# Kernel tuning notes

Hardware: AMD Instinct MI355X
Metric: run time of the kernel (lower is better)

## Reference

```python
import jax, jax.numpy as jnp
import numpy as np

T, B, N = 1000, 64, 512
DT = 0.01
EL, VR, TR, TINF = -0.07, -0.07, -0.06, -0.05
A_VAL = 2.6239240169525146
A1_VAL = -0.015625353902578354
A2_VAL = -1.0590057373046875
B_VAL = 12.77495288848877
G_VAL = 45.24007797241211
K1, K2 = 200.0, 20.0
R1, R2 = 0.3858567178249359, -1.1421641111373901
C = 1.0


def setup_inputs() -> dict:
    key = jax.random.key(0)
    x = jax.random.normal(key, (T, B, N), dtype=jnp.float32)
    linear = jnp.ones((1, N), jnp.float32)
    a = jnp.full((1, N), A_VAL, jnp.float32)
    A1 = jnp.full((1, N), A1_VAL * C, jnp.float32)
    A2 = jnp.full((1, N), A2_VAL * C, jnp.float32)
    return {"x": x, "linear": linear, "a": a, "A1": A1, "A2": A2}


def _spike(v):
    # Heaviside step (forward of SurrGradSpike)
    return (v > 0).astype(v.dtype)


def reference(x, linear, a, A1, A2):
    G = G_VAL * C

    def step(state, xt):
        V, i1, i2, Thr = state
        i1 = i1 - K1 * i1 * DT
        i2 = i2 - K2 * i2 * DT
        V = V + DT * (linear * xt + i1 + i2 - G * (V - EL)) / C
        Thr = Thr + DT * (a * (V - EL) - B_VAL * (Thr - TINF))
        spk = _spike(V - Thr)
        i1 = (1.0 - spk) * i1 + spk * (R1 * i1 + A1)
        i2 = (1.0 - spk) * i2 + spk * (R2 * i2 + A2)
        Thr = (1.0 - spk) * Thr + spk * jnp.maximum(Thr, TR)
        V = (1.0 - spk) * V + spk * VR
        return (V, i1, i2, Thr), spk

    Bd, Nd = x.shape[1], x.shape[2]
    init = (
        jnp.full((Bd, Nd), EL, x.dtype),   # V
        jnp.zeros((Bd, Nd), x.dtype),      # i1
        jnp.zeros((Bd, Nd), x.dtype),      # i2
        jnp.full((Bd, Nd), TINF, x.dtype), # Thr
    )
    _, spikes = jax.lax.scan(step, init, x)
    return spikes  # [T, B, N] (original returns np.array of per-step spikes)
```

## Files before the change

kernel.cpp:

```cpp
#include <hip/hip_runtime.h>


#define T_STEPS 1000
#define B_DIM 64
#define N_DIM 512
#define BN (B_DIM * N_DIM)

#define K_CHUNK 20
#define NCHUNK (T_STEPS / K_CHUNK)

typedef const __attribute__((address_space(1))) void* gp_t;
typedef __attribute__((address_space(3))) void* lp_t;
typedef float f32x4 __attribute__((ext_vector_type(4)));

__device__ __forceinline__ void raw_barrier() {
    asm volatile("s_barrier" ::: "memory");
}

struct Consts {
    float k200, k20, kDT, kEL, kG, kTINF, kB, kR1, kR2, kTR;
};

__device__ __forceinline__ float mn_step_spec(
    float xt, float lin, float av, float A1v, float A2v, const Consts& K,
    float& V1, float& T1, float& tm_,
    float& i1d, float& i1r, float& i2d, float& i2r, bool& sbp)
{
#pragma clang fp contract(off)
    float a1n = i1d - (K.k200 * i1d) * K.kDT;
    float a1s = i1r - (K.k200 * i1r) * K.kDT;
    float a2n = i2d - (K.k20  * i2d) * K.kDT;
    float a2s = i2r - (K.k20  * i2r) * K.kDT;
    float p   = lin * xt;
    float qn  = p + a1n;
    float qs  = p + a1s;
    float rn  = qn + a2n;
    float rs  = qs + a2s;
    float en  = V1 - K.kEL;
    float gn  = K.kG * en;
    float sn  = rn - gn;
    float dn  = K.kDT * sn;
    float dsp = K.kDT * rs;
    float Vn  = V1 + dn;
    float Vs  = K.kEL + dsp;
    float e2n = Vn - K.kEL;
    float e2s = Vs - K.kEL;
    float un  = av * e2n;
    float us  = av * e2s;
    float wn  = T1  - K.kTINF;
    float ws  = tm_ - K.kTINF;
    float bn  = K.kB * wn;
    float bs  = K.kB * ws;
    float s2n = un - bn;
    float s2s = us - bs;
    float d2n = K.kDT * s2n;
    float d2s = K.kDT * s2s;
    float T1n = T1  + d2n;
    float T1s = tm_ + d2s;
    float dfn = Vn - T1n;
    float dfs = Vs - T1s;
    float diff = sbp ? dfs : dfn;
    V1  = sbp ? Vs  : Vn;
    T1  = sbp ? T1s : T1n;
    i1d = sbp ? a1s : a1n;
    i2d = sbp ? a2s : a2n;
    bool  sb  = diff > 0.0f;
    float spk = sb ? 1.0f : 0.0f;
    sbp = sb;
    tm_ = fmaxf(T1, K.kTR);
    i1r = (K.kR1 * i1d) + A1v;
    i2r = (K.kR2 * i2d) + A2v;
    return spk;
}

__global__ __launch_bounds__(128, 1) void mn_neuron_kernel(
    const float* __restrict__ x, const float* __restrict__ linear,
    const float* __restrict__ a, const float* __restrict__ A1,
    const float* __restrict__ A2, float* __restrict__ out)
{
#pragma clang fp contract(off)
    __shared__ float xb_buf[2][K_CHUNK][64];
    __shared__ float sb_buf[2][K_CHUNK][64];

    const int lane = threadIdx.x & 63;
    const int wid  = threadIdx.x >> 6;
    const int blk  = blockIdx.x;

    if (wid == 1) {
        const float* pl = x + (size_t)(lane >> 4) * BN
                            + (size_t)blk * 64 + (size_t)(lane & 15) * 4;
        float* outp = out + (size_t)blk * 64;

        auto issue = [&](int k) {
            const float* pc = pl + (size_t)(k * K_CHUNK) * BN;
            float* dst = &xb_buf[k & 1][0][0];
#pragma unroll
            for (int s5 = 0; s5 < K_CHUNK / 4; ++s5) {
                __builtin_amdgcn_global_load_lds(
                    (gp_t)(pc + (size_t)(s5 * 4) * BN),
                    (lp_t)(dst + s5 * 4 * 64), 16, 0, 0);
            }
        };

        const int r0 = lane >> 4;
        const int c4 = (lane & 15) * 4;
        auto flush = [&](int k) {
            const int kb = k & 1;
#pragma unroll
            for (int pz = 0; pz < K_CHUNK / 4; ++pz) {
                const int row = pz * 4 + r0;
                const f32x4 v = *reinterpret_cast<const f32x4*>(
                    &sb_buf[kb][row][c4]);
                f32x4* dp = reinterpret_cast<f32x4*>(
                    outp + (size_t)(k * K_CHUNK + row) * BN + c4);
                __builtin_nontemporal_store(v, dp);
            }
        };

        issue(0);
        asm volatile("s_waitcnt vmcnt(0)" ::: "memory");
        raw_barrier();

        for (int c = 0; c < NCHUNK; ++c) {
            if (c + 1 < NCHUNK) issue(c + 1);
            if (c >= 1)         flush(c - 1);
            asm volatile("s_waitcnt vmcnt(0) lgkmcnt(0)" ::: "memory");
            raw_barrier();
        }
        flush(NCHUNK - 1);
    } else {
        const int idx = blk * 64 + lane;
        const int n   = idx & (N_DIM - 1);

        const float lin = linear[n];
        const float av  = a[n];
        const float A1v = A1[n];
        const float A2v = A2[n];

        Consts K = {200.0f, 20.0f, 0.01f, -0.07f,
                    45.24007797241211f, -0.05f, 12.77495288848877f,
                    0.3858567178249359f, -1.1421641111373901f, -0.06f};
        asm volatile("" : "+s"(K.k200), "+s"(K.k20), "+s"(K.kDT),
                          "+s"(K.kEL), "+s"(K.kG), "+s"(K.kTINF),
                          "+s"(K.kB), "+s"(K.kR1), "+s"(K.kR2), "+s"(K.kTR));

        float V1  = K.kEL;
        float T1  = K.kTINF;
        float tm_ = fmaxf(K.kTINF, K.kTR);
        float i1d = 0.0f;
        float i1r = (K.kR1 * 0.0f) + A1v;
        float i2d = 0.0f;
        float i2r = (K.kR2 * 0.0f) + A2v;
        bool  sbp = false;

        asm volatile("s_setprio 1" ::: "memory");
        raw_barrier();

        for (int c = 0; c < NCHUNK; ++c) {
            const float* src = &xb_buf[c & 1][0][lane];
            float*       dst = &sb_buf[c & 1][0][lane];
#pragma unroll
            for (int j = 0; j < K_CHUNK; ++j) {
                float xt  = src[j * 64];
                float spk = mn_step_spec(xt, lin, av, A1v, A2v, K,
                                         V1, T1, tm_, i1d, i1r, i2d, i2r, sbp);
                dst[j * 64] = spk;
            }
            asm volatile("s_waitcnt lgkmcnt(0)" ::: "memory");
            raw_barrier();
        }
    }
}

extern "C" void kernel_launch(void* const* d_in, const int* in_sizes, int n_in,
                              void* d_out, int out_size, void* d_ws, size_t ws_size,
                              hipStream_t stream) {
    const float* x      = (const float*)d_in[0];
    const float* linear = (const float*)d_in[1];
    const float* a      = (const float*)d_in[2];
    const float* A1     = (const float*)d_in[3];
    const float* A2     = (const float*)d_in[4];
    float* out = (float*)d_out;

    mn_neuron_kernel<<<BN / 64, 128, 0, stream>>>(x, linear, a, A1, A2, out);
}
```

Baseline: 246.8 us.

## Deepen x prefetch to four buffers and restructure speculative step recurrence

The producer wave now keeps three chunks of x in flight across a four-slot LDS ring, using partial vmcnt waits instead of draining all loads every chunk. The compute wave's step is reorganized so both spike/no-spike branches for the next step are integrated right after the select, with the next x value preloaded (including across chunk boundaries). This aims to shorten the serial dependency chain per timestep and hide global load latency. It adds LDS usage and relies on careful vmcnt counting at the tail. The initial step now reads xb_buf[0] after the first barrier, which depends on the first chunk having landed.

```diff
diff --git a/kernel.cpp b/kernel.cpp
--- a/kernel.cpp
+++ b/kernel.cpp
@@ -8,6 +8,7 @@
 
 #define K_CHUNK 20
 #define NCHUNK (T_STEPS / K_CHUNK)
+#define NBUF 4
 
 typedef const __attribute__((address_space(1))) void* gp_t;
 typedef __attribute__((address_space(3))) void* lp_t;
@@ -21,55 +22,76 @@
     float k200, k20, kDT, kEL, kG, kTINF, kB, kR1, kR2, kTR;
 };
 
-__device__ __forceinline__ float mn_step_spec(
-    float xt, float lin, float av, float A1v, float A2v, const Consts& K,
-    float& V1, float& T1, float& tm_,
-    float& i1d, float& i1r, float& i2d, float& i2r, bool& sbp)
+struct Pairs {
+    float Vn, Vs;
+    float Tn, Ts;
+    float i1n, i1s;
+    float i2n, i2s;
+    bool  cn, cs;
+};
+
+__device__ __forceinline__ Pairs dual_integrate(
+    float xt, float lin, float av, const Consts& K,
+    float Vin, float i1nin, float i2nin, float Tnin,
+    float i1sin, float i2sin, float Tsin)
 {
 #pragma clang fp contract(off)
-    float a1n = i1d - (K.k200 * i1d) * K.kDT;
-    float a1s = i1r - (K.k200 * i1r) * K.kDT;
-    float a2n = i2d - (K.k20  * i2d) * K.kDT;
-    float a2s = i2r - (K.k20  * i2r) * K.kDT;
+    Pairs P;
     float p   = lin * xt;
+    float a1n = i1nin - (K.k200 * i1nin) * K.kDT;
+    float a2n = i2nin - (K.k20  * i2nin) * K.kDT;
     float qn  = p + a1n;
-    float qs  = p + a1s;
     float rn  = qn + a2n;
-    float rs  = qs + a2s;
-    float en  = V1 - K.kEL;
+    float en  = Vin - K.kEL;
     float gn  = K.kG * en;
     float sn  = rn - gn;
     float dn  = K.kDT * sn;
-    float dsp = K.kDT * rs;
-    float Vn  = V1 + dn;
-    float Vs  = K.kEL + dsp;
-    float e2n = Vn - K.kEL;
-    float e2s = Vs - K.kEL;
+    float Vpn = Vin + dn;
+    float e2n = Vpn - K.kEL;
     float un  = av * e2n;
+    float wn  = Tnin - K.kTINF;
+    float bwn = K.kB * wn;
+    float s2n = un - bwn;
+    float d2n = K.kDT * s2n;
+    float Tpn = Tnin + d2n;
+    float a1s = i1sin - (K.k200 * i1sin) * K.kDT;
+    float a2s = i2sin - (K.k20  * i2sin) * K.kDT;
+    float qs  = p + a1s;
+    float rs  = qs + a2s;
+    float ds  = K.kDT * rs;
+    float Vps = K.kEL + ds;
+    float e2s = Vps - K.kEL;
     float us  = av * e2s;
-    float wn  = T1  - K.kTINF;
-    float ws  = tm_ - K.kTINF;
-    float bn  = K.kB * wn;
-    float bs  = K.kB * ws;
-    float s2n = un - bn;
-    float s2s = us - bs;
-    float d2n = K.kDT * s2n;
+    float ws  = Tsin - K.kTINF;
+    float bws = K.kB * ws;
+    float s2s = us - bws;
     float d2s = K.kDT * s2s;
-    float T1n = T1  + d2n;
-    float T1s = tm_ + d2s;
-    float dfn = Vn - T1n;
-    float dfs = Vs - T1s;
-    float diff = sbp ? dfs : dfn;
-    V1  = sbp ? Vs  : Vn;
-    T1  = sbp ? T1s : T1n;
-    i1d = sbp ? a1s : a1n;
-    i2d = sbp ? a2s : a2n;
-    bool  sb  = diff > 0.0f;
+    float Tps = Tsin + d2s;
+    P.Vn = Vpn; P.Vs = Vps; P.Tn = Tpn; P.Ts = Tps;
+    P.i1n = a1n; P.i1s = a1s; P.i2n = a2n; P.i2s = a2s;
+    P.cn = Vpn > Tpn;
+    P.cs = Vps > Tps;
+    return P;
+}
+
+__device__ __forceinline__ float resolve_and_advance(
+    float xt1, float lin, float av, float A1v, float A2v, const Consts& K,
+    Pairs& P, bool& sbp)
+{
+#pragma clang fp contract(off)
+    bool  sb  = sbp ? P.cs : P.cn;
     float spk = sb ? 1.0f : 0.0f;
+    float V1  = sbp ? P.Vs  : P.Vn;
+    float T1  = sbp ? P.Ts  : P.Tn;
+    float i1d = sbp ? P.i1s : P.i1n;
+    float i2d = sbp ? P.i2s : P.i2n;
+    float i1r  = (K.kR1 * i1d) + A1v;
+    float i2r  = (K.kR2 * i2d) + A2v;
+    float tmax = fmaxf(T1, K.kTR);
+    P = dual_integrate(xt1, lin, av, K,
+                       V1, i1d, i2d, T1,
+                       i1r, i2r, tmax);
     sbp = sb;
-    tm_ = fmaxf(T1, K.kTR);
-    i1r = (K.kR1 * i1d) + A1v;
-    i2r = (K.kR2 * i2d) + A2v;
     return spk;
 }
 
@@ -79,7 +101,7 @@
     const float* __restrict__ A2, float* __restrict__ out)
 {
 #pragma clang fp contract(off)
-    __shared__ float xb_buf[2][K_CHUNK][64];
+    __shared__ float xb_buf[NBUF][K_CHUNK][64];
     __shared__ float sb_buf[2][K_CHUNK][64];
 
     const int lane = threadIdx.x & 63;
@@ -93,7 +115,7 @@
 
         auto issue = [&](int k) {
             const float* pc = pl + (size_t)(k * K_CHUNK) * BN;
-            float* dst = &xb_buf[k & 1][0][0];
+            float* dst = &xb_buf[k & (NBUF - 1)][0][0];
 #pragma unroll
             for (int s5 = 0; s5 < K_CHUNK / 4; ++s5) {
                 __builtin_amdgcn_global_load_lds(
@@ -117,14 +139,19 @@
             }
         };
 
-        issue(0);
-        asm volatile("s_waitcnt vmcnt(0)" ::: "memory");
+        issue(0); issue(1); issue(2);
+        asm volatile("s_waitcnt vmcnt(5)" ::: "memory");
         raw_barrier();
 
         for (int c = 0; c < NCHUNK; ++c) {
-            if (c + 1 < NCHUNK) issue(c + 1);
-            if (c >= 1)         flush(c - 1);
-            asm volatile("s_waitcnt vmcnt(0) lgkmcnt(0)" ::: "memory");
+            if (c + 3 < NCHUNK) issue(c + 3);
+            if (c <= NCHUNK - 4) {
+                asm volatile("s_waitcnt vmcnt(5)" ::: "memory");
+            } else {
+                asm volatile("s_waitcnt vmcnt(0)" ::: "memory");
+            }
+            if (c >= 1) flush(c - 1);
+            asm volatile("s_waitcnt lgkmcnt(0)" ::: "memory");
             raw_barrier();
         }
         flush(NCHUNK - 1);
@@ -144,26 +171,27 @@
                           "+s"(K.kEL), "+s"(K.kG), "+s"(K.kTINF),
                           "+s"(K.kB), "+s"(K.kR1), "+s"(K.kR2), "+s"(K.kTR));
 
-        float V1  = K.kEL;
-        float T1  = K.kTINF;
-        float tm_ = fmaxf(K.kTINF, K.kTR);
-        float i1d = 0.0f;
-        float i1r = (K.kR1 * 0.0f) + A1v;
-        float i2d = 0.0f;
-        float i2r = (K.kR2 * 0.0f) + A2v;
-        bool  sbp = false;
-
         asm volatile("s_setprio 1" ::: "memory");
         raw_barrier();
 
+        bool  sbp = false;
+        Pairs P;
+        {
+            float x0 = xb_buf[0][0][lane];
+            P = dual_integrate(x0, lin, av, K,
+                               K.kEL, 0.0f, 0.0f, K.kTINF,
+                               0.0f, 0.0f, K.kTINF);
+        }
+
         for (int c = 0; c < NCHUNK; ++c) {
-            const float* src = &xb_buf[c & 1][0][lane];
+            const float* src = &xb_buf[c & (NBUF - 1)][0][lane];
+            const float* nxt = &xb_buf[(c + 1) & (NBUF - 1)][0][lane];
             float*       dst = &sb_buf[c & 1][0][lane];
 #pragma unroll
             for (int j = 0; j < K_CHUNK; ++j) {
-                float xt  = src[j * 64];
-                float spk = mn_step_spec(xt, lin, av, A1v, A2v, K,
-                                         V1, T1, tm_, i1d, i1r, i2d, i2r, sbp);
+                float xt1 = (j < K_CHUNK - 1) ? src[(j + 1) * 64] : nxt[0];
+                float spk = resolve_and_advance(xt1, lin, av, A1v, A2v, K,
+                                                P, sbp);
                 dst[j * 64] = spk;
             }
             asm volatile("s_waitcnt lgkmcnt(0)" ::: "memory");
```

Result: slower. 254.6 us (+3.2%).
